# Optimization experiments

Measured on AMD Instinct MI355X. Metric: run time of the kernel, lower is better.

The kernel has to match this reference:

```python
import jax, jax.numpy as jnp
import numpy as np

N_STEPS = 16   # fixed-step RK4 steps over t in [0, 1]
T0, T1 = 0.0, 1.0


def setup_inputs() -> dict:
    key = jax.random.key(0)
    k = jax.random.split(key, 5)
    B, D, H = 1024, 512, 2048
    x = jax.random.normal(k[0], (B, D), dtype=jnp.float32)
    W1 = jax.random.normal(k[1], (D, H), dtype=jnp.float32) / np.float32(np.sqrt(D))
    b1 = jnp.zeros((H,), dtype=jnp.float32)
    W2 = jax.random.normal(k[2], (H, D), dtype=jnp.float32) / np.float32(np.sqrt(H))
    b2 = jnp.zeros((D,), dtype=jnp.float32)
    return {"x": x, "W1": W1, "b1": b1, "W2": W2, "b2": b2}


def reference(x, W1, b1, W2, b2):
    # odefunc: time-conditioned 2-layer MLP, f(t, y) has same shape as y
    def f(t, y):
        h = jnp.tanh(y @ W1 + b1 + t)   # [B, H]
        return h @ W2 + b2              # [B, D]

    dt = jnp.float32((T1 - T0) / N_STEPS)
    half = jnp.float32(0.5)
    sixth = jnp.float32(1.0 / 6.0)

    def step(y, t):
        k1 = f(t, y)
        k2 = f(t + half * dt, y + half * dt * k1)
        k3 = f(t + half * dt, y + half * dt * k2)
        k4 = f(t + dt, y + dt * k3)
        y_next = y + dt * sixth * (k1 + 2.0 * k2 + 2.0 * k3 + k4)
        return y_next, None

    ts = jnp.float32(T0) + dt * jnp.arange(N_STEPS, dtype=jnp.float32)
    y1, _ = jax.lax.scan(step, x, ts)
    # ODEBlock returns out[1] (state at t=1) cast to float32
    return y1.astype(jnp.float32)
```

## Files before the change

kernel.cpp:

```cpp
#include <hip/hip_runtime.h>
#include <cstdint>


typedef __bf16 bf16x8 __attribute__((ext_vector_type(8)));
typedef float f32x4 __attribute__((ext_vector_type(4)));

#define AS1 __attribute__((address_space(1)))
#define AS3 __attribute__((address_space(3)))

#define MDIM 1024
#define DDIM 512
#define HDIM 2048

#define GEMM_LDS (64 * 1024)
#define GEMM2_LDS (64 * 1024)

__device__ __forceinline__ void async_copy16(const void* g, void* lds) {
  __builtin_amdgcn_global_load_lds((const AS1 void*)g, (AS3 void*)lds, 16, 0, 0);
}

__device__ __forceinline__ unsigned short f32_to_bf16(float f) {
  union { float f; unsigned u; } c; c.f = f;
  unsigned u = c.u + 0x7FFFu + ((c.u >> 16) & 1u);
  return (unsigned short)(u >> 16);
}

__device__ __forceinline__ unsigned char f32_to_fp8(float v) {
  unsigned p;
  asm("v_cvt_pk_fp8_f32 %0, %1, %1" : "=v"(p) : "v"(v));
  return (unsigned char)(p & 0xFF);
}

__device__ __forceinline__ float tanh_fast(float x) {
  float a = __builtin_fabsf(x);
  float e = __expf(-2.0f * a);
  float r = (1.0f - e) * __builtin_amdgcn_rcpf(1.0f + e);
  return __builtin_copysignf(r, x);
}

__global__ __launch_bounds__(256) void transpose_bf16_kernel(
    const float* __restrict__ in, unsigned short* __restrict__ out, int R, int C) {
  __shared__ float tile[64][65];
  int nbc = C >> 6;
  int br = blockIdx.x / nbc, bc = blockIdx.x % nbc;
  int r0 = br * 64, c0 = bc * 64;
  int tr = threadIdx.x >> 6, tc = threadIdx.x & 63;
  for (int i = 0; i < 16; ++i) {
    int row = i * 4 + tr;
    tile[row][tc] = in[(r0 + row) * C + c0 + tc];
  }
  __syncthreads();
  for (int i = 0; i < 16; ++i) {
    int row = i * 4 + tr;
    out[(c0 + row) * R + r0 + tc] = f32_to_bf16(tile[tc][row]);
  }
}

__global__ __launch_bounds__(256) void transpose_fp8_kernel(
    const float* __restrict__ in, unsigned char* __restrict__ out, int R, int C) {
  __shared__ float tile[64][65];
  int nbc = C >> 6;
  int br = blockIdx.x / nbc, bc = blockIdx.x % nbc;
  int r0 = br * 64, c0 = bc * 64;
  int tr = threadIdx.x >> 6, tc = threadIdx.x & 63;
  for (int i = 0; i < 16; ++i) {
    int row = i * 4 + tr;
    tile[row][tc] = in[(r0 + row) * C + c0 + tc];
  }
  __syncthreads();
  for (int i = 0; i < 16; ++i) {
    int row = i * 4 + tr;
    out[(c0 + row) * R + r0 + tc] = f32_to_fp8(tile[tc][row]);
  }
}

__global__ __launch_bounds__(256) void init_kernel(
    const float* __restrict__ x, float* __restrict__ y,
    unsigned short* __restrict__ arg) {
  int i = blockIdx.x * 256 + threadIdx.x;
  float v = x[i];
  y[i] = v;
  arg[i] = f32_to_bf16(v);
}

__global__ __launch_bounds__(256, 2) void gemm1_kernel(
    const unsigned short* __restrict__ A,
    const unsigned short* __restrict__ Bt,
    const float* __restrict__ b1, float tval,
    unsigned char* __restrict__ H8)
{
  extern __shared__ char ldsbuf[];
  bf16x8* sA = (bf16x8*)ldsbuf;
  bf16x8* sB = (bf16x8*)(ldsbuf + 32768);
  const int K = DDIM;
  const int NITER = 4;
  int bid = blockIdx.x;
  int lid = (bid & 7) * 64 + (bid >> 3);
  int bn = lid >> 4;
  int bm = lid & 15;
  int tid = threadIdx.x;
  int lane = tid & 63;
  int wid = tid >> 6;
  int l15 = lane & 15;
  int l4 = lane >> 4;
  int wm = (wid >> 1) * 32;
  int wn = (wid & 1) * 32;
  int sw = l15 & 7;

  const unsigned short* gA[4];
  const unsigned short* gB[4];
#pragma unroll
  for (int i = 0; i < 4; ++i) {
    int u = tid + i * 256, r = u >> 4, s = u & 15;
    int koff = ((s ^ (r & 7)) * 8);
    gA[i] = A + (size_t)(bm * 64 + r) * K + koff;
    gB[i] = Bt + (size_t)(bn * 64 + r) * K + koff;
  }
  f32x4 acc[2][2] = {};

#pragma unroll
  for (int i = 0; i < 4; ++i) {
    async_copy16(gA[i], &sA[tid + i * 256]);
    async_copy16(gB[i], &sB[tid + i * 256]);
  }

#pragma unroll 1
  for (int kt = 0; kt < NITER; ++kt) {
    int cur = kt & 1;
    __syncthreads();
    if (kt + 1 < NITER) {
      int nxt = cur ^ 1;
      int off = (kt + 1) * 128;
#pragma unroll
      for (int i = 0; i < 4; ++i) {
        async_copy16(gA[i] + off, &sA[nxt * 1024 + tid + i * 256]);
        async_copy16(gB[i] + off, &sB[nxt * 1024 + tid + i * 256]);
      }
    }
#pragma unroll
    for (int ks = 0; ks < 4; ++ks) {
      int kg = (ks * 4 + l4) ^ sw;
      bf16x8 af[2], bfr[2];
#pragma unroll
      for (int i = 0; i < 2; ++i)
        af[i] = sA[cur * 1024 + (wm + i * 16 + l15) * 16 + kg];
#pragma unroll
      for (int j = 0; j < 2; ++j)
        bfr[j] = sB[cur * 1024 + (wn + j * 16 + l15) * 16 + kg];
#pragma unroll
      for (int i = 0; i < 2; ++i)
#pragma unroll
        for (int j = 0; j < 2; ++j)
          acc[i][j] = __builtin_amdgcn_mfma_f32_16x16x32_bf16(
              af[i], bfr[j], acc[i][j], 0, 0, 0);
    }
  }
  int row0 = bm * 64 + wm + l4 * 4;
  int col0 = bn * 64 + wn + l15;
  float bias[2];
  for (int j = 0; j < 2; ++j) bias[j] = b1[col0 + j * 16] + tval;
#pragma unroll
  for (int i = 0; i < 2; ++i)
#pragma unroll
    for (int r = 0; r < 4; ++r) {
      unsigned char* Hrow = H8 + (size_t)(row0 + i * 16 + r) * HDIM + col0;
      Hrow[0]  = f32_to_fp8(tanh_fast(acc[i][0][r] + bias[0]));
      Hrow[16] = f32_to_fp8(tanh_fast(acc[i][1][r] + bias[1]));
    }
}

__global__ __launch_bounds__(256, 2) void gemm2rk4_kernel(
    const unsigned char* __restrict__ A8,
    const unsigned char* __restrict__ B8,
    const float* __restrict__ b2,
    float* __restrict__ y, float* __restrict__ kacc,
    unsigned short* __restrict__ arg, int mode, float dt)
{
  extern __shared__ char ldsbuf[];
  char* sA8 = ldsbuf;
  char* sB8 = ldsbuf + 32768;
  const int K = HDIM;
  int bid = blockIdx.x;
  int lid = (bid & 7) * 64 + (bid >> 3);
  int bm = lid >> 4;
  int bn = lid & 15;
  int tid = threadIdx.x;
  int lane = tid & 63;
  int wid = tid >> 6;
  int l15 = lane & 15;
  int l4 = lane >> 4;
  int sw = l15 & 7;

  const unsigned char* gA[4];
  const unsigned char* gB[4];
#pragma unroll
  for (int i = 0; i < 4; ++i) {
    int u = tid + i * 256;
    int w = u >> 8, r = (u >> 3) & 31, sl = u & 7;
    int koff = w * 512 + ((sl ^ (r & 7)) * 16);
    gA[i] = A8 + (size_t)(bm * 32 + r) * K + koff;
    gB[i] = B8 + (size_t)(bn * 32 + r) * K + koff;
  }
  f32x4 acc[2][2] = {};

#pragma unroll
  for (int i = 0; i < 4; ++i) {
    async_copy16(gA[i], sA8 + (tid + i * 256) * 16);
    async_copy16(gB[i], sB8 + (tid + i * 256) * 16);
  }

#pragma unroll 1
  for (int kt = 0; kt < 4; ++kt) {
    int cur = kt & 1;
    __syncthreads();
    if (kt + 1 < 4) {
      int nxt = cur ^ 1;
      int off = (kt + 1) * 128;
#pragma unroll
      for (int i = 0; i < 4; ++i) {
        async_copy16(gA[i] + off, sA8 + nxt * 16384 + (tid + i * 256) * 16);
        async_copy16(gB[i] + off, sB8 + nxt * 16384 + (tid + i * 256) * 16);
      }
    }
#pragma unroll
    for (int ks = 0; ks < 4; ++ks) {
      int soff = (((ks * 2 + (l4 >> 1)) ^ sw) * 16) + (l4 & 1) * 8;
      long af[2], bfr[2];
#pragma unroll
      for (int i = 0; i < 2; ++i)
        af[i] = *(const long*)(sA8 + cur * 16384 + wid * 4096 +
                               (i * 16 + l15) * 128 + soff);
#pragma unroll
      for (int j = 0; j < 2; ++j)
        bfr[j] = *(const long*)(sB8 + cur * 16384 + wid * 4096 +
                                (j * 16 + l15) * 128 + soff);
#pragma unroll
      for (int i = 0; i < 2; ++i)
#pragma unroll
        for (int j = 0; j < 2; ++j)
          acc[i][j] = __builtin_amdgcn_mfma_f32_16x16x32_fp8_fp8(
              af[i], bfr[j], acc[i][j], 0, 0, 0);
    }
  }

  __syncthreads();
  float* red = (float*)ldsbuf;
#pragma unroll
  for (int i = 0; i < 2; ++i)
#pragma unroll
    for (int j = 0; j < 2; ++j)
#pragma unroll
      for (int q = 0; q < 4; ++q) {
        int row = i * 16 + l4 * 4 + q;
        int col = j * 16 + l15;
        red[(wid * 32 + row) * 36 + col] = acc[i][j][q];
      }
  __syncthreads();

  int row = tid >> 3;
  int c4 = (tid & 7) * 4;
  float4 s0 = *(float4*)&red[(0 * 32 + row) * 36 + c4];
  float4 s1 = *(float4*)&red[(1 * 32 + row) * 36 + c4];
  float4 s2 = *(float4*)&red[(2 * 32 + row) * 36 + c4];
  float4 s3 = *(float4*)&red[(3 * 32 + row) * 36 + c4];
  int grow = bm * 32 + row;
  int gcol = bn * 32 + c4;
  size_t off = (size_t)grow * DDIM + gcol;
  float4 bb = *(const float4*)(b2 + gcol);
  float4 k;
  k.x = s0.x + s1.x + s2.x + s3.x + bb.x;
  k.y = s0.y + s1.y + s2.y + s3.y + bb.y;
  k.z = s0.z + s1.z + s2.z + s3.z + bb.z;
  k.w = s0.w + s1.w + s2.w + s3.w + bb.w;
  float4 yv = *(const float4*)(y + off);
  float hh = 0.5f * dt;
  float sx = dt * (1.0f / 6.0f);
  float4 argv;
  if (mode == 0) {
    *(float4*)(kacc + off) = k;
    argv.x = yv.x + hh * k.x; argv.y = yv.y + hh * k.y;
    argv.z = yv.z + hh * k.z; argv.w = yv.w + hh * k.w;
  } else if (mode == 1) {
    float4 ka = *(const float4*)(kacc + off);
    ka.x += 2.0f * k.x; ka.y += 2.0f * k.y; ka.z += 2.0f * k.z; ka.w += 2.0f * k.w;
    *(float4*)(kacc + off) = ka;
    argv.x = yv.x + hh * k.x; argv.y = yv.y + hh * k.y;
    argv.z = yv.z + hh * k.z; argv.w = yv.w + hh * k.w;
  } else if (mode == 2) {
    float4 ka = *(const float4*)(kacc + off);
    ka.x += 2.0f * k.x; ka.y += 2.0f * k.y; ka.z += 2.0f * k.z; ka.w += 2.0f * k.w;
    *(float4*)(kacc + off) = ka;
    argv.x = yv.x + dt * k.x; argv.y = yv.y + dt * k.y;
    argv.z = yv.z + dt * k.z; argv.w = yv.w + dt * k.w;
  } else {
    float4 ka = *(const float4*)(kacc + off);
    argv.x = yv.x + sx * (ka.x + k.x); argv.y = yv.y + sx * (ka.y + k.y);
    argv.z = yv.z + sx * (ka.z + k.z); argv.w = yv.w + sx * (ka.w + k.w);
    *(float4*)(y + off) = argv;
  }
  ushort4 av;
  av.x = f32_to_bf16(argv.x); av.y = f32_to_bf16(argv.y);
  av.z = f32_to_bf16(argv.z); av.w = f32_to_bf16(argv.w);
  *(ushort4*)(arg + off) = av;
}

extern "C" void kernel_launch(void* const* d_in, const int* in_sizes, int n_in,
                              void* d_out, int out_size, void* d_ws, size_t ws_size,
                              hipStream_t stream) {
  (void)in_sizes; (void)n_in; (void)out_size; (void)ws_size;
  const float* x  = (const float*)d_in[0];
  const float* W1 = (const float*)d_in[1];
  const float* b1 = (const float*)d_in[2];
  const float* W2 = (const float*)d_in[3];
  const float* b2 = (const float*)d_in[4];
  float* y = (float*)d_out;

  char* ws = (char*)d_ws;
  unsigned short* W1T  = (unsigned short*)(ws);
  unsigned char*  W2T8 = (unsigned char*)(ws + (2u << 20));
  unsigned char*  H8   = (unsigned char*)(ws + (4u << 20));
  unsigned short* arg  = (unsigned short*)(ws + (8u << 20));
  float*          kacc = (float*)(ws + (9u << 20));

  hipFuncSetAttribute((const void*)gemm1_kernel,
                      hipFuncAttributeMaxDynamicSharedMemorySize, GEMM_LDS);
  hipFuncSetAttribute((const void*)gemm2rk4_kernel,
                      hipFuncAttributeMaxDynamicSharedMemorySize, GEMM2_LDS);

  transpose_bf16_kernel<<<256, 256, 0, stream>>>(W1, W1T, DDIM, HDIM);
  transpose_fp8_kernel<<<256, 256, 0, stream>>>(W2, W2T8, HDIM, DDIM);
  init_kernel<<<MDIM * DDIM / 256, 256, 0, stream>>>(x, y, arg);

  const float dt = 1.0f / 16.0f;
  for (int n = 0; n < 16; ++n) {
    float t0 = dt * (float)n;
    const float ts[4] = {t0, t0 + 0.5f * dt, t0 + 0.5f * dt, t0 + dt};
    for (int s = 0; s < 4; ++s) {
      gemm1_kernel<<<512, 256, GEMM_LDS, stream>>>(arg, W1T, b1, ts[s], H8);
      gemm2rk4_kernel<<<512, 256, GEMM2_LDS, stream>>>(H8, W2T8, b2, y, kacc, arg, s, dt);
    }
  }
}
```

Before: 876.9 us.

## Drop GEMM double buffering to halve LDS and raise occupancy; fuse setup kernels

Both GEMM kernels now use a single-buffered 32 KB LDS tile instead of double-buffered 64 KB, with a sync before and after each async load, and their launch bounds go from 2 to 4 blocks per CU. The aim is more resident blocks to hide latency in place of software prefetch. The cost is that loads and MFMA work no longer overlap within a block. Separately, the two weight transposes and the init kernel are merged into one setup launch to save two launch overheads.

```diff
diff --git a/kernel.cpp b/kernel.cpp
--- a/kernel.cpp
+++ b/kernel.cpp
@@ -12,8 +12,8 @@
 #define DDIM 512
 #define HDIM 2048
 
-#define GEMM_LDS (64 * 1024)
-#define GEMM2_LDS (64 * 1024)
+#define GEMM_LDS (32 * 1024)
+#define GEMM2_LDS (32 * 1024)
 
 __device__ __forceinline__ void async_copy16(const void* g, void* lds) {
   __builtin_amdgcn_global_load_lds((const AS1 void*)g, (AS3 void*)lds, 16, 0, 0);
@@ -38,52 +38,47 @@
   return __builtin_copysignf(r, x);
 }
 
-__global__ __launch_bounds__(256) void transpose_bf16_kernel(
-    const float* __restrict__ in, unsigned short* __restrict__ out, int R, int C) {
+__global__ __launch_bounds__(256) void setup_kernel(
+    const float* __restrict__ x, float* __restrict__ y,
+    unsigned short* __restrict__ arg,
+    const float* __restrict__ W1, unsigned short* __restrict__ W1T,
+    const float* __restrict__ W2, unsigned char* __restrict__ W2T8) {
   __shared__ float tile[64][65];
-  int nbc = C >> 6;
-  int br = blockIdx.x / nbc, bc = blockIdx.x % nbc;
-  int r0 = br * 64, c0 = bc * 64;
-  int tr = threadIdx.x >> 6, tc = threadIdx.x & 63;
-  for (int i = 0; i < 16; ++i) {
-    int row = i * 4 + tr;
-    tile[row][tc] = in[(r0 + row) * C + c0 + tc];
-  }
-  __syncthreads();
-  for (int i = 0; i < 16; ++i) {
-    int row = i * 4 + tr;
-    out[(c0 + row) * R + r0 + tc] = f32_to_bf16(tile[tc][row]);
-  }
-}
-
-__global__ __launch_bounds__(256) void transpose_fp8_kernel(
-    const float* __restrict__ in, unsigned char* __restrict__ out, int R, int C) {
-  __shared__ float tile[64][65];
-  int nbc = C >> 6;
-  int br = blockIdx.x / nbc, bc = blockIdx.x % nbc;
-  int r0 = br * 64, c0 = bc * 64;
-  int tr = threadIdx.x >> 6, tc = threadIdx.x & 63;
-  for (int i = 0; i < 16; ++i) {
-    int row = i * 4 + tr;
-    tile[row][tc] = in[(r0 + row) * C + c0 + tc];
-  }
-  __syncthreads();
-  for (int i = 0; i < 16; ++i) {
-    int row = i * 4 + tr;
-    out[(c0 + row) * R + r0 + tc] = f32_to_fp8(tile[tc][row]);
-  }
-}
-
-__global__ __launch_bounds__(256) void init_kernel(
-    const float* __restrict__ x, float* __restrict__ y,
-    unsigned short* __restrict__ arg) {
-  int i = blockIdx.x * 256 + threadIdx.x;
-  float v = x[i];
-  y[i] = v;
-  arg[i] = f32_to_bf16(v);
-}
-
-__global__ __launch_bounds__(256, 2) void gemm1_kernel(
+  int b = blockIdx.x;
+  if (b < 512) {
+    const float* in = (b < 256) ? W1 : W2;
+    int R = (b < 256) ? DDIM : HDIM;
+    int C = (b < 256) ? HDIM : DDIM;
+    int bb = b & 255;
+    int nbc = C >> 6;
+    int br = bb / nbc, bc = bb % nbc;
+    int r0 = br * 64, c0 = bc * 64;
+    int tr = threadIdx.x >> 6, tc = threadIdx.x & 63;
+    for (int i = 0; i < 16; ++i) {
+      int row = i * 4 + tr;
+      tile[row][tc] = in[(r0 + row) * C + c0 + tc];
+    }
+    __syncthreads();
+    if (b < 256) {
+      for (int i = 0; i < 16; ++i) {
+        int row = i * 4 + tr;
+        W1T[(c0 + row) * R + r0 + tc] = f32_to_bf16(tile[tc][row]);
+      }
+    } else {
+      for (int i = 0; i < 16; ++i) {
+        int row = i * 4 + tr;
+        W2T8[(c0 + row) * R + r0 + tc] = f32_to_fp8(tile[tc][row]);
+      }
+    }
+  } else {
+    int i = (b - 512) * 256 + threadIdx.x;
+    float v = x[i];
+    y[i] = v;
+    arg[i] = f32_to_bf16(v);
+  }
+}
+
+__global__ __launch_bounds__(256, 4) void gemm1_kernel(
     const unsigned short* __restrict__ A,
     const unsigned short* __restrict__ Bt,
     const float* __restrict__ b1, float tval,
@@ -91,9 +86,8 @@
 {
   extern __shared__ char ldsbuf[];
   bf16x8* sA = (bf16x8*)ldsbuf;
-  bf16x8* sB = (bf16x8*)(ldsbuf + 32768);
+  bf16x8* sB = (bf16x8*)(ldsbuf + 16384);
   const int K = DDIM;
-  const int NITER = 4;
   int bid = blockIdx.x;
   int lid = (bid & 7) * 64 + (bid >> 3);
   int bn = lid >> 4;
@@ -118,35 +112,26 @@
   }
   f32x4 acc[2][2] = {};
 
-#pragma unroll
-  for (int i = 0; i < 4; ++i) {
-    async_copy16(gA[i], &sA[tid + i * 256]);
-    async_copy16(gB[i], &sB[tid + i * 256]);
-  }
-
 #pragma unroll 1
-  for (int kt = 0; kt < NITER; ++kt) {
-    int cur = kt & 1;
-    __syncthreads();
-    if (kt + 1 < NITER) {
-      int nxt = cur ^ 1;
-      int off = (kt + 1) * 128;
-#pragma unroll
-      for (int i = 0; i < 4; ++i) {
-        async_copy16(gA[i] + off, &sA[nxt * 1024 + tid + i * 256]);
-        async_copy16(gB[i] + off, &sB[nxt * 1024 + tid + i * 256]);
-      }
-    }
+  for (int kt = 0; kt < 4; ++kt) {
+    int off = kt * 128;
+    __syncthreads();
+#pragma unroll
+    for (int i = 0; i < 4; ++i) {
+      async_copy16(gA[i] + off, &sA[tid + i * 256]);
+      async_copy16(gB[i] + off, &sB[tid + i * 256]);
+    }
+    __syncthreads();
 #pragma unroll
     for (int ks = 0; ks < 4; ++ks) {
       int kg = (ks * 4 + l4) ^ sw;
       bf16x8 af[2], bfr[2];
 #pragma unroll
       for (int i = 0; i < 2; ++i)
-        af[i] = sA[cur * 1024 + (wm + i * 16 + l15) * 16 + kg];
+        af[i] = sA[(wm + i * 16 + l15) * 16 + kg];
 #pragma unroll
       for (int j = 0; j < 2; ++j)
-        bfr[j] = sB[cur * 1024 + (wn + j * 16 + l15) * 16 + kg];
+        bfr[j] = sB[(wn + j * 16 + l15) * 16 + kg];
 #pragma unroll
       for (int i = 0; i < 2; ++i)
 #pragma unroll
@@ -169,7 +154,7 @@
     }
 }
 
-__global__ __launch_bounds__(256, 2) void gemm2rk4_kernel(
+__global__ __launch_bounds__(256, 4) void gemm2rk4_kernel(
     const unsigned char* __restrict__ A8,
     const unsigned char* __restrict__ B8,
     const float* __restrict__ b2,
@@ -178,7 +163,7 @@
 {
   extern __shared__ char ldsbuf[];
   char* sA8 = ldsbuf;
-  char* sB8 = ldsbuf + 32768;
+  char* sB8 = ldsbuf + 16384;
   const int K = HDIM;
   int bid = blockIdx.x;
   int lid = (bid & 7) * 64 + (bid >> 3);
@@ -203,37 +188,26 @@
   }
   f32x4 acc[2][2] = {};
 
-#pragma unroll
-  for (int i = 0; i < 4; ++i) {
-    async_copy16(gA[i], sA8 + (tid + i * 256) * 16);
-    async_copy16(gB[i], sB8 + (tid + i * 256) * 16);
-  }
-
 #pragma unroll 1
   for (int kt = 0; kt < 4; ++kt) {
-    int cur = kt & 1;
-    __syncthreads();
-    if (kt + 1 < 4) {
-      int nxt = cur ^ 1;
-      int off = (kt + 1) * 128;
-#pragma unroll
-      for (int i = 0; i < 4; ++i) {
-        async_copy16(gA[i] + off, sA8 + nxt * 16384 + (tid + i * 256) * 16);
-        async_copy16(gB[i] + off, sB8 + nxt * 16384 + (tid + i * 256) * 16);
-      }
-    }
+    int off = kt * 128;
+    __syncthreads();
+#pragma unroll
+    for (int i = 0; i < 4; ++i) {
+      async_copy16(gA[i] + off, sA8 + (tid + i * 256) * 16);
+      async_copy16(gB[i] + off, sB8 + (tid + i * 256) * 16);
+    }
+    __syncthreads();
 #pragma unroll
     for (int ks = 0; ks < 4; ++ks) {
       int soff = (((ks * 2 + (l4 >> 1)) ^ sw) * 16) + (l4 & 1) * 8;
       long af[2], bfr[2];
 #pragma unroll
       for (int i = 0; i < 2; ++i)
-        af[i] = *(const long*)(sA8 + cur * 16384 + wid * 4096 +
-                               (i * 16 + l15) * 128 + soff);
+        af[i] = *(const long*)(sA8 + wid * 4096 + (i * 16 + l15) * 128 + soff);
 #pragma unroll
       for (int j = 0; j < 2; ++j)
-        bfr[j] = *(const long*)(sB8 + cur * 16384 + wid * 4096 +
-                                (j * 16 + l15) * 128 + soff);
+        bfr[j] = *(const long*)(sB8 + wid * 4096 + (j * 16 + l15) * 128 + soff);
 #pragma unroll
       for (int i = 0; i < 2; ++i)
 #pragma unroll
@@ -327,9 +301,7 @@
   hipFuncSetAttribute((const void*)gemm2rk4_kernel,
                       hipFuncAttributeMaxDynamicSharedMemorySize, GEMM2_LDS);
 
-  transpose_bf16_kernel<<<256, 256, 0, stream>>>(W1, W1T, DDIM, HDIM);
-  transpose_fp8_kernel<<<256, 256, 0, stream>>>(W2, W2T8, HDIM, DDIM);
-  init_kernel<<<MDIM * DDIM / 256, 256, 0, stream>>>(x, y, arg);
+  setup_kernel<<<2560, 256, 0, stream>>>(x, y, arg, W1, W1T, W2, W2T8);
 
   const float dt = 1.0f / 16.0f;
   for (int n = 0; n < 16; ++n) {
```

Result: slower. 977.0 us (+11.4%).
